# Performance work log

Hardware: AMD Instinct MI355X
Metric: run time of the kernel (lower is better)

The kernel has to match this reference:

```python
import jax, jax.numpy as jnp
import numpy as np

EMB = 1024
HEADS = 16
HEADSIZE = EMB // HEADS
EPS = 1e-5  # torch LayerNorm default


def _layernorm(x, g, b):
    # normalize over last dim (headsize)
    m = jnp.mean(x, axis=-1, keepdims=True)
    v = jnp.mean((x - m) ** 2, axis=-1, keepdims=True)
    return (x - m) * jax.lax.rsqrt(v + EPS) * g + b


def setup_inputs() -> dict:
    key = jax.random.key(0)
    ks = jax.random.split(key, 6)
    B, T = 4, 2048
    s = 1.0 / np.sqrt(EMB)  # ~ torch Linear init scale
    return {
        "x": jax.random.normal(ks[0], (B, T, EMB), dtype=jnp.float32),
        "Wk": jax.random.normal(ks[1], (EMB, EMB), dtype=jnp.float32) * s,
        "Wq": jax.random.normal(ks[2], (EMB, EMB), dtype=jnp.float32) * s,
        "Wv": jax.random.normal(ks[3], (EMB, EMB), dtype=jnp.float32) * s,
        "Wo": jax.random.normal(ks[4], (EMB, EMB), dtype=jnp.float32) * s,
        "bo": jnp.zeros((EMB,), dtype=jnp.float32),
        "kln_g": jnp.ones((HEADSIZE,), dtype=jnp.float32),
        "kln_b": jnp.zeros((HEADSIZE,), dtype=jnp.float32),
        "qln_g": jnp.ones((HEADSIZE,), dtype=jnp.float32),
        "qln_b": jnp.zeros((HEADSIZE,), dtype=jnp.float32),
    }


def reference(x, Wk, Wq, Wv, Wo, bo, kln_g, kln_b, qln_g, qln_b):
    B, T, E = x.shape
    # projections (torch Linear: y = x @ W.T), split into heads
    k = jnp.einsum("bte,fe->btf", x, Wk).reshape(B, T, HEADS, HEADSIZE)
    q = jnp.einsum("bte,fe->btf", x, Wq).reshape(B, T, HEADS, HEADSIZE)
    v = jnp.einsum("bte,fe->btf", x, Wv).reshape(B, T, HEADS, HEADSIZE)
    # optional per-head layernorm on keys/queries (kqnorm=True)
    k = _layernorm(k, kln_g, kln_b)
    q = _layernorm(q, qln_g, qln_b)
    # note: original scales by emb**-1/4 on each of q and k (total 1/sqrt(emb))
    scale = E ** (-0.25)
    q = q * scale
    k = k * scale
    # full [B, H, T, T] score matrix (faithful to bmm implementation)
    dot = jnp.einsum("bihd,bjhd->bhij", q, k)
    # causal mask: j > i set to -inf (mask_diagonal=False -> offset=1)
    causal = jnp.triu(jnp.ones((T, T), dtype=bool), k=1)
    dot = jnp.where(causal, -jnp.inf, dot)
    att = jax.nn.softmax(dot, axis=-1)
    out = jnp.einsum("bhij,bjhd->bihd", att, v).reshape(B, T, E)
    return jnp.einsum("bte,fe->btf", out, Wo) + bo
```

## Files before the change

kernel.cpp:

```cpp
#include <hip/hip_runtime.h>
#include <hip/hip_bf16.h>
#include <cstdint>

#define EMB 1024
#define HEADS 16
#define HD 64
#define BATCH 4
#define SEQ 2048
#define BT (BATCH*SEQ)
#define LNEPS 1e-5f
#define QK_SCALE 0.17677669529663687f
#define LOG2E 1.4426950408889634f

typedef __bf16 bf16;
typedef __bf16 bf16x8 __attribute__((ext_vector_type(8)));
typedef __bf16 bf16x4 __attribute__((ext_vector_type(4)));
typedef float  f32x4  __attribute__((ext_vector_type(4)));
typedef short  s16x4  __attribute__((ext_vector_type(4)));

typedef const __attribute__((address_space(1))) void* gas_ptr;
typedef __attribute__((address_space(3))) void*       las_ptr;

__device__ __forceinline__ void gld_lds16(const void* g, void* l) {
  __builtin_amdgcn_global_load_lds((gas_ptr)g, (las_ptr)l, 16, 0, 0);
}

__device__ __forceinline__ f32x4 mfma_pv(bf16x4 a, bf16x4 b, f32x4 c) {
  return __builtin_amdgcn_mfma_f32_16x16x16bf16_1k(
      __builtin_bit_cast(s16x4, a), __builtin_bit_cast(s16x4, b), c, 0, 0, 0);
}

__global__ void cvt_all(const float* __restrict__ x,
                        const float* __restrict__ w0, const float* __restrict__ w1,
                        const float* __restrict__ w2, const float* __restrict__ w3,
                        bf16* __restrict__ xb, bf16* __restrict__ wb) {
  const int bid = blockIdx.x;
  if (bid < 8192) {
    int i = bid * 256 + threadIdx.x;
    float4 f = reinterpret_cast<const float4*>(x)[i];
    bf16x4 o = { (bf16)f.x, (bf16)f.y, (bf16)f.z, (bf16)f.w };
    reinterpret_cast<bf16x4*>(xb)[i] = o;
  } else {
    int i = (bid - 8192) * 256 + threadIdx.x;
    int sel = i >> 18;
    int j = i & 262143;
    const float* s = (sel == 0) ? w0 : (sel == 1) ? w1 : (sel == 2) ? w2 : w3;
    float4 f = reinterpret_cast<const float4*>(s)[j];
    bf16x4 o = { (bf16)f.x, (bf16)f.y, (bf16)f.z, (bf16)f.w };
    reinterpret_cast<bf16x4*>(wb)[i] = o;
  }
}

__global__ __launch_bounds__(256, 2) void gemm_kqv(
    const bf16* __restrict__ A, const bf16* __restrict__ Bm,
    bf16* __restrict__ kn, bf16* __restrict__ qn, bf16* __restrict__ vt,
    const float* __restrict__ kg, const float* __restrict__ kb,
    const float* __restrict__ qg, const float* __restrict__ qb)
{
  __shared__ __align__(16) bf16 As[128 * 32];
  __shared__ __align__(16) bf16 Bs[128 * 32];

  const int K = EMB;
  const int t    = threadIdx.x;
  const int lane = t & 63;
  const int wave = t >> 6;
  const int q    = lane >> 4;
  const int ln   = lane & 15;

  const int lid = (int)blockIdx.y * (int)gridDim.x + (int)blockIdx.x;
  const int xcd = lid & 7;
  const int nn  = lid >> 3;
  const int bxr = nn >> 3;
  const int byr = (xcd << 3) | (nn & 7);
  const int m0  = byr * 128;
  const int n0  = bxr * 128;

  const int wm = (wave >> 1) * 64;
  const int wn = (wave & 1) * 64;

  const int r0 = t >> 2;
  const int c0 = (t & 3) << 3;

  f32x4 zero4 = {0.f, 0.f, 0.f, 0.f};
  f32x4 acc[4][4];
#pragma unroll
  for (int i = 0; i < 4; i++)
#pragma unroll
    for (int j = 0; j < 4; j++) acc[i][j] = zero4;

  for (int k0 = 0; k0 < K; k0 += 32) {
    __syncthreads();
    const bf16* ga = A  + (size_t)(m0 + r0) * K + k0 + c0;
    const bf16* gb = Bm + (size_t)(n0 + r0) * K + k0 + c0;
    gld_lds16(ga,                  &As[t * 8]);
    gld_lds16(ga + (size_t)64 * K, &As[t * 8 + 2048]);
    gld_lds16(gb,                  &Bs[t * 8]);
    gld_lds16(gb + (size_t)64 * K, &Bs[t * 8 + 2048]);
    __syncthreads();

    bf16x8 af[4], bfr[4];
#pragma unroll
    for (int mi = 0; mi < 4; mi++)
      af[mi] = *reinterpret_cast<const bf16x8*>(&As[(wm + mi * 16 + ln) * 32 + q * 8]);
#pragma unroll
    for (int ni = 0; ni < 4; ni++)
      bfr[ni] = *reinterpret_cast<const bf16x8*>(&Bs[(wn + ni * 16 + ln) * 32 + q * 8]);
#pragma unroll
    for (int mi = 0; mi < 4; mi++)
#pragma unroll
      for (int ni = 0; ni < 4; ni++)
        acc[mi][ni] = __builtin_amdgcn_mfma_f32_16x16x32_bf16(af[mi], bfr[ni], acc[mi][ni], 0, 0, 0);
  }

  const int sec = n0 >> 10;
  const int cb  = (n0 & 1023) + wn;
  const int h   = cb >> 6;
  const int R0  = m0 + wm;

  if (sec == 2) {
#pragma unroll
    for (int mi = 0; mi < 4; mi++) {
      const int R = R0 + mi * 16 + q * 4;
      const int b = R >> 11, tt = R & 2047;
#pragma unroll
      for (int ni = 0; ni < 4; ni++) {
        const int d = ni * 16 + ln;
        bf16x4 o4 = { (bf16)acc[mi][ni][0], (bf16)acc[mi][ni][1],
                      (bf16)acc[mi][ni][2], (bf16)acc[mi][ni][3] };
        *reinterpret_cast<bf16x4*>(
            &vt[((size_t)(b * HEADS + h) * HD + d) * SEQ + tt]) = o4;
      }
    }
  } else {
    const float scale = sec ? QK_SCALE : (QK_SCALE * LOG2E);
    const float* gp = sec ? qg : kg;
    const float* bp = sec ? qb : kb;
    bf16* outp = sec ? qn : kn;
    float gv[4], bv[4];
#pragma unroll
    for (int ni = 0; ni < 4; ni++) {
      gv[ni] = gp[ni * 16 + ln];
      bv[ni] = bp[ni * 16 + ln] * scale;
    }
#pragma unroll
    for (int mi = 0; mi < 4; mi++) {
#pragma unroll
      for (int r = 0; r < 4; r++) {
        const float x0 = acc[mi][0][r], x1 = acc[mi][1][r];
        const float x2 = acc[mi][2][r], x3 = acc[mi][3][r];
        float s  = (x0 + x1) + (x2 + x3);
        float s2 = (x0 * x0 + x1 * x1) + (x2 * x2 + x3 * x3);
#pragma unroll
        for (int mm = 1; mm < 16; mm <<= 1) {
          s  += __shfl_xor(s,  mm, 64);
          s2 += __shfl_xor(s2, mm, 64);
        }
        const float mean = s * (1.f / 64.f);
        const float rs = rsqrtf(s2 * (1.f / 64.f) - mean * mean + LNEPS) * scale;
        const int R = R0 + mi * 16 + q * 4 + r;
        const int b = R >> 11, tt = R & 2047;
        const size_t o = ((size_t)(b * HEADS + h) * SEQ + tt) * HD + ln;
#pragma unroll
        for (int ni = 0; ni < 4; ni++)
          outp[o + ni * 16] = (bf16)((acc[mi][ni][r] - mean) * rs * gv[ni] + bv[ni]);
      }
    }
  }
}

template<int OUTF32>
__global__ __launch_bounds__(256, 2) void gemm_bt(
    const bf16* __restrict__ A, const bf16* __restrict__ Bm,
    bf16* __restrict__ Cb, float* __restrict__ Cf, const float* __restrict__ bias,
    int M, int N, int K)
{
  __shared__ __align__(16) bf16 As[128 * 32];
  __shared__ __align__(16) bf16 Bs[128 * 32];

  const int t    = threadIdx.x;
  const int lane = t & 63;
  const int wave = t >> 6;
  const int q    = lane >> 4;
  const int ln   = lane & 15;

  const int lid = (int)blockIdx.y * (int)gridDim.x + (int)blockIdx.x;
  const int xcd = lid & 7;
  const int nn  = lid >> 3;
  const int bxr = nn >> 3;
  const int byr = (xcd << 3) | (nn & 7);
  const int m0  = byr * 128;
  const int n0  = bxr * 128;

  const int wm   = (wave >> 1) * 64;
  const int wn   = (wave & 1) * 64;

  const int r0 = t >> 2;
  const int c0 = (t & 3) << 3;

  f32x4 zero4 = {0.f, 0.f, 0.f, 0.f};
  f32x4 acc[4][4];
#pragma unroll
  for (int i = 0; i < 4; i++)
#pragma unroll
    for (int j = 0; j < 4; j++) acc[i][j] = zero4;

  for (int k0 = 0; k0 < K; k0 += 32) {
    __syncthreads();
    const bf16* ga = A  + (size_t)(m0 + r0) * K + k0 + c0;
    const bf16* gb = Bm + (size_t)(n0 + r0) * K + k0 + c0;
    gld_lds16(ga,                  &As[t * 8]);
    gld_lds16(ga + (size_t)64 * K, &As[t * 8 + 2048]);
    gld_lds16(gb,                  &Bs[t * 8]);
    gld_lds16(gb + (size_t)64 * K, &Bs[t * 8 + 2048]);
    __syncthreads();

    bf16x8 af[4], bfr[4];
#pragma unroll
    for (int mi = 0; mi < 4; mi++)
      af[mi] = *reinterpret_cast<const bf16x8*>(&As[(wm + mi * 16 + ln) * 32 + q * 8]);
#pragma unroll
    for (int ni = 0; ni < 4; ni++)
      bfr[ni] = *reinterpret_cast<const bf16x8*>(&Bs[(wn + ni * 16 + ln) * 32 + q * 8]);
#pragma unroll
    for (int mi = 0; mi < 4; mi++)
#pragma unroll
      for (int ni = 0; ni < 4; ni++)
        acc[mi][ni] = __builtin_amdgcn_mfma_f32_16x16x32_bf16(af[mi], bfr[ni], acc[mi][ni], 0, 0, 0);
  }

#pragma unroll
  for (int mi = 0; mi < 4; mi++) {
#pragma unroll
    for (int ni = 0; ni < 4; ni++) {
#pragma unroll
      for (int r = 0; r < 4; r++) {
        int row = m0 + wm + mi * 16 + q * 4 + r;
        int col = n0 + wn + ni * 16 + ln;
        float v = acc[mi][ni][r];
        if (OUTF32) Cf[(size_t)row * N + col] = v + bias[col];
        else        Cb[(size_t)row * N + col] = (bf16)v;
      }
    }
  }
}

__global__ __launch_bounds__(256, 4) void attn(
    const bf16* __restrict__ Qn, const bf16* __restrict__ Kn, const bf16* __restrict__ Vt,
    bf16* __restrict__ O)
{
  __shared__ __align__(16) bf16 Ks[2][64 * 64];
  __shared__ __align__(16) bf16 Vs[2][64 * 64];

  const int id = blockIdx.x;
  const int bh = ((id >> 7) << 3) | (id & 7);
  const int bxi = (id >> 3) & 15;
  const int t = threadIdx.x, wave = t >> 6, lane = t & 63;
  const int q = lane >> 4, ln = lane & 15;
  const int b = bh >> 4, h = bh & 15;

  const int u0 = t * 8, u1 = t * 8 + 2048;
  const int kr0 = u0 >> 6, kc0 = ((u0 >> 3) & 7) ^ (kr0 & 7);
  const int kr1 = u1 >> 6, kc1 = ((u1 >> 3) & 7) ^ (kr1 & 7);
  const int vd0 = u0 >> 6, vc0 = ((u0 >> 3) & 7) ^ (vd0 & 7);
  const int vd1 = u1 >> 6, vc1 = ((u1 >> 3) & 7) ^ (vd1 & 7);
  const bf16* Kb = Kn + (size_t)bh * SEQ * HD;
  const bf16* Vb = Vt + (size_t)bh * HD * SEQ;

  f32x4 zero4 = {0.f, 0.f, 0.f, 0.f};

  for (int pass = 0; pass < 2; ++pass) {
    const int itile = pass ? (31 - bxi) : bxi;
    const int qbase = itile * 64 + wave * 16;

    const bf16* qp = Qn + ((size_t)bh * SEQ + qbase + ln) * HD + q * 8;
    bf16x8 qf0 = *reinterpret_cast<const bf16x8*>(qp);
    bf16x8 qf1 = *reinterpret_cast<const bf16x8*>(qp + 32);

    float lrow = 0.f;
    f32x4 oacc[4];
#pragma unroll
    for (int md = 0; md < 4; md++) oacc[md] = zero4;

    const int nj = itile + 1;

    __syncthreads();
    {
      gld_lds16(Kb + (size_t)kr0 * HD + kc0 * 8, &Ks[0][u0]);
      gld_lds16(Kb + (size_t)kr1 * HD + kc1 * 8, &Ks[0][u1]);
      gld_lds16(Vb + (size_t)vd0 * SEQ + vc0 * 8, &Vs[0][u0]);
      gld_lds16(Vb + (size_t)vd1 * SEQ + vc1 * 8, &Vs[0][u1]);
    }

    for (int jt = 0; jt < nj; ++jt) {
      const int buf = jt & 1;
      const int j0 = jt * 64;
      __syncthreads();
      if (jt + 1 < nj) {
        const int jn = j0 + 64;
        gld_lds16(Kb + (size_t)(jn + kr0) * HD + kc0 * 8, &Ks[buf ^ 1][u0]);
        gld_lds16(Kb + (size_t)(jn + kr1) * HD + kc1 * 8, &Ks[buf ^ 1][u1]);
        gld_lds16(Vb + (size_t)vd0 * SEQ + jn + vc0 * 8, &Vs[buf ^ 1][u0]);
        gld_lds16(Vb + (size_t)vd1 * SEQ + jn + vc1 * 8, &Vs[buf ^ 1][u1]);
      }

#pragma unroll
      for (int jb = 0; jb < 4; ++jb) {
        const int jslab = j0 + jb * 16;
        if (jslab <= qbase + 15) {
          const int rowj = jb * 16 + ln;
          bf16x8 kf0 = *reinterpret_cast<const bf16x8*>(
              &Ks[buf][rowj * 64 + ((q)     ^ (rowj & 7)) * 8]);
          bf16x8 kf1 = *reinterpret_cast<const bf16x8*>(
              &Ks[buf][rowj * 64 + ((4 + q) ^ (rowj & 7)) * 8]);
          f32x4 z = zero4;
          z = __builtin_amdgcn_mfma_f32_16x16x32_bf16(kf0, qf0, z, 0, 0, 0);
          z = __builtin_amdgcn_mfma_f32_16x16x32_bf16(kf1, qf1, z, 0, 0, 0);
          if (jslab + 15 > qbase) {
#pragma unroll
            for (int r = 0; r < 4; r++) {
              int jj = jslab + q * 4 + r;
              int ii = qbase + ln;
              if (jj > ii) z[r] = -1.0e30f;
            }
          }
          float p0 = exp2f(z[0]), p1 = exp2f(z[1]), p2 = exp2f(z[2]), p3 = exp2f(z[3]);
          lrow += (p0 + p1) + (p2 + p3);
          bf16x4 pk = { (bf16)p0, (bf16)p1, (bf16)p2, (bf16)p3 };

#pragma unroll
          for (int md = 0; md < 4; md++) {
            const int rowd = md * 16 + ln;
            const bf16* vp = &Vs[buf][rowd * 64 +
                (((jb * 2 + (q >> 1)) ^ (rowd & 7)) * 8) + (q & 1) * 4];
            bf16x4 vf = *reinterpret_cast<const bf16x4*>(vp);
            oacc[md] = mfma_pv(vf, pk, oacc[md]);
          }
        }
      }
    }

    float s = lrow;
    s += __shfl_xor(s, 16, 64);
    s += __shfl_xor(s, 32, 64);
    const float inv = 1.f / s;
    const int row = qbase + ln;
#pragma unroll
    for (int md = 0; md < 4; md++) {
      bf16x4 o4 = { (bf16)(oacc[md][0] * inv), (bf16)(oacc[md][1] * inv),
                    (bf16)(oacc[md][2] * inv), (bf16)(oacc[md][3] * inv) };
      int col = h * HD + md * 16 + q * 4;
      *reinterpret_cast<bf16x4*>(&O[(size_t)(b * SEQ + row) * EMB + col]) = o4;
    }
  }
}

extern "C" void kernel_launch(void* const* d_in, const int* in_sizes, int n_in,
                              void* d_out, int out_size, void* d_ws, size_t ws_size,
                              hipStream_t stream)
{
  const float* x   = (const float*)d_in[0];
  const float* Wk  = (const float*)d_in[1];
  const float* Wq  = (const float*)d_in[2];
  const float* Wv  = (const float*)d_in[3];
  const float* Wo  = (const float*)d_in[4];
  const float* bo  = (const float*)d_in[5];
  const float* klg = (const float*)d_in[6];
  const float* klb = (const float*)d_in[7];
  const float* qlg = (const float*)d_in[8];
  const float* qlb = (const float*)d_in[9];
  float* out = (float*)d_out;

  char* ws = (char*)d_ws;
  const size_t OFF_XB  = 0;
  const size_t OFF_WB  = OFF_XB  + (size_t)BT * EMB * 2;
  const size_t OFF_KQV = OFF_WB  + (size_t)4 * EMB * EMB * 2;
  const size_t OFF_KN  = OFF_KQV + (size_t)BT * 3 * EMB * 2;
  const size_t OFF_QN  = OFF_KN  + (size_t)BT * EMB * 2;
  const size_t OFF_VT  = OFF_QN  + (size_t)BT * EMB * 2;
  const size_t OFF_END = OFF_VT  + (size_t)BT * EMB * 2;
  if (ws_size < OFF_END) return;

  bf16* xb   = (bf16*)(ws + OFF_XB);
  bf16* wb   = (bf16*)(ws + OFF_WB);
  bf16* kn   = (bf16*)(ws + OFF_KN);
  bf16* qn   = (bf16*)(ws + OFF_QN);
  bf16* vt   = (bf16*)(ws + OFF_VT);
  bf16* ob   = (bf16*)(ws + OFF_KQV);

  cvt_all<<<12288, 256, 0, stream>>>(x, Wk, Wq, Wv, Wo, xb, wb);

  gemm_kqv<<<dim3(3 * EMB / 128, BT / 128), 256, 0, stream>>>(
      xb, wb, kn, qn, vt, klg, klb, qlg, qlb);

  attn<<<dim3(16 * BATCH * HEADS), 256, 0, stream>>>(qn, kn, vt, ob);

  gemm_bt<1><<<dim3(EMB / 128, BT / 128), 256, 0, stream>>>(
      ob, wb + (size_t)3 * EMB * EMB, (bf16*)nullptr, out, bo, BT, EMB, EMB);
}
```

Measured before the change: 267.2 us.

## Double-buffer GEMM K-loop with 64-wide swizzled LDS tiles

Both projection GEMMs now share a macro that double-buffers LDS tiles, prefetching the next K tile with global_load_lds while MFMAs run on the current one, and needs only one barrier per iteration. The K tile grows from 32 to 64 and the LDS layout uses an XOR swizzle on 16-byte chunks to avoid bank conflicts on fragment reads. The goal is to hide global load latency and cut barrier and LDS-conflict overhead. LDS use rises to 64KB per block, which may limit occupancy to one block per CU and reduce latency hiding across blocks.

```diff
diff --git a/kernel.cpp b/kernel.cpp
--- a/kernel.cpp
+++ b/kernel.cpp
@@ -51,16 +51,70 @@
   }
 }
 
+#define GEMM_DBUF_LOOP(A_, B_, K_)                                            \
+  f32x4 zero4 = {0.f, 0.f, 0.f, 0.f};                                         \
+  f32x4 acc[4][4];                                                            \
+  _Pragma("unroll")                                                           \
+  for (int i = 0; i < 4; i++)                                                 \
+    _Pragma("unroll")                                                         \
+    for (int j = 0; j < 4; j++) acc[i][j] = zero4;                            \
+  {                                                                           \
+    _Pragma("unroll")                                                         \
+    for (int i = 0; i < 4; i++) {                                             \
+      const int u = t * 8 + i * 2048;                                         \
+      const int row = u >> 6;                                                 \
+      const int c = ((u >> 3) & 7) ^ (row & 7);                               \
+      gld_lds16(A_ + (size_t)(m0 + row) * K_ + c * 8, &As[0][u]);             \
+      gld_lds16(B_ + (size_t)(n0 + row) * K_ + c * 8, &Bs[0][u]);             \
+    }                                                                         \
+  }                                                                           \
+  for (int kt = 0; kt < K_ / 64; ++kt) {                                      \
+    const int buf = kt & 1;                                                   \
+    __syncthreads();                                                          \
+    if (kt + 1 < K_ / 64) {                                                   \
+      const int k0 = (kt + 1) * 64;                                           \
+      _Pragma("unroll")                                                       \
+      for (int i = 0; i < 4; i++) {                                           \
+        const int u = t * 8 + i * 2048;                                       \
+        const int row = u >> 6;                                               \
+        const int c = ((u >> 3) & 7) ^ (row & 7);                             \
+        gld_lds16(A_ + (size_t)(m0 + row) * K_ + k0 + c * 8, &As[buf^1][u]);  \
+        gld_lds16(B_ + (size_t)(n0 + row) * K_ + k0 + c * 8, &Bs[buf^1][u]);  \
+      }                                                                       \
+    }                                                                         \
+    _Pragma("unroll")                                                         \
+    for (int ks = 0; ks < 2; ++ks) {                                          \
+      bf16x8 af[4], bfr[4];                                                   \
+      _Pragma("unroll")                                                       \
+      for (int mi = 0; mi < 4; mi++) {                                        \
+        const int row = wm + mi * 16 + ln;                                    \
+        af[mi] = *reinterpret_cast<const bf16x8*>(                            \
+            &As[buf][row * 64 + ((ks * 4 + q) ^ (row & 7)) * 8]);             \
+      }                                                                       \
+      _Pragma("unroll")                                                       \
+      for (int ni = 0; ni < 4; ni++) {                                        \
+        const int row = wn + ni * 16 + ln;                                    \
+        bfr[ni] = *reinterpret_cast<const bf16x8*>(                           \
+            &Bs[buf][row * 64 + ((ks * 4 + q) ^ (row & 7)) * 8]);             \
+      }                                                                       \
+      _Pragma("unroll")                                                       \
+      for (int mi = 0; mi < 4; mi++)                                          \
+        _Pragma("unroll")                                                     \
+        for (int ni = 0; ni < 4; ni++)                                        \
+          acc[mi][ni] = __builtin_amdgcn_mfma_f32_16x16x32_bf16(              \
+              af[mi], bfr[ni], acc[mi][ni], 0, 0, 0);                         \
+    }                                                                         \
+  }
+
 __global__ __launch_bounds__(256, 2) void gemm_kqv(
     const bf16* __restrict__ A, const bf16* __restrict__ Bm,
     bf16* __restrict__ kn, bf16* __restrict__ qn, bf16* __restrict__ vt,
     const float* __restrict__ kg, const float* __restrict__ kb,
     const float* __restrict__ qg, const float* __restrict__ qb)
 {
-  __shared__ __align__(16) bf16 As[128 * 32];
-  __shared__ __align__(16) bf16 Bs[128 * 32];
-
-  const int K = EMB;
+  __shared__ __align__(16) bf16 As[2][128 * 64];
+  __shared__ __align__(16) bf16 Bs[2][128 * 64];
+
   const int t    = threadIdx.x;
   const int lane = t & 63;
   const int wave = t >> 6;
@@ -78,39 +132,7 @@
   const int wm = (wave >> 1) * 64;
   const int wn = (wave & 1) * 64;
 
-  const int r0 = t >> 2;
-  const int c0 = (t & 3) << 3;
-
-  f32x4 zero4 = {0.f, 0.f, 0.f, 0.f};
-  f32x4 acc[4][4];
-#pragma unroll
-  for (int i = 0; i < 4; i++)
-#pragma unroll
-    for (int j = 0; j < 4; j++) acc[i][j] = zero4;
-
-  for (int k0 = 0; k0 < K; k0 += 32) {
-    __syncthreads();
-    const bf16* ga = A  + (size_t)(m0 + r0) * K + k0 + c0;
-    const bf16* gb = Bm + (size_t)(n0 + r0) * K + k0 + c0;
-    gld_lds16(ga,                  &As[t * 8]);
-    gld_lds16(ga + (size_t)64 * K, &As[t * 8 + 2048]);
-    gld_lds16(gb,                  &Bs[t * 8]);
-    gld_lds16(gb + (size_t)64 * K, &Bs[t * 8 + 2048]);
-    __syncthreads();
-
-    bf16x8 af[4], bfr[4];
-#pragma unroll
-    for (int mi = 0; mi < 4; mi++)
-      af[mi] = *reinterpret_cast<const bf16x8*>(&As[(wm + mi * 16 + ln) * 32 + q * 8]);
-#pragma unroll
-    for (int ni = 0; ni < 4; ni++)
-      bfr[ni] = *reinterpret_cast<const bf16x8*>(&Bs[(wn + ni * 16 + ln) * 32 + q * 8]);
-#pragma unroll
-    for (int mi = 0; mi < 4; mi++)
-#pragma unroll
-      for (int ni = 0; ni < 4; ni++)
-        acc[mi][ni] = __builtin_amdgcn_mfma_f32_16x16x32_bf16(af[mi], bfr[ni], acc[mi][ni], 0, 0, 0);
-  }
+  GEMM_DBUF_LOOP(A, Bm, EMB)
 
   const int sec = n0 >> 10;
   const int cb  = (n0 & 1023) + wn;
@@ -168,14 +190,12 @@
   }
 }
 
-template<int OUTF32>
-__global__ __launch_bounds__(256, 2) void gemm_bt(
+__global__ __launch_bounds__(256, 2) void gemm_out(
     const bf16* __restrict__ A, const bf16* __restrict__ Bm,
-    bf16* __restrict__ Cb, float* __restrict__ Cf, const float* __restrict__ bias,
-    int M, int N, int K)
+    float* __restrict__ Cf, const float* __restrict__ bias, int N)
 {
-  __shared__ __align__(16) bf16 As[128 * 32];
-  __shared__ __align__(16) bf16 Bs[128 * 32];
+  __shared__ __align__(16) bf16 As[2][128 * 64];
+  __shared__ __align__(16) bf16 Bs[2][128 * 64];
 
   const int t    = threadIdx.x;
   const int lane = t & 63;
@@ -191,42 +211,10 @@
   const int m0  = byr * 128;
   const int n0  = bxr * 128;
 
-  const int wm   = (wave >> 1) * 64;
-  const int wn   = (wave & 1) * 64;
-
-  const int r0 = t >> 2;
-  const int c0 = (t & 3) << 3;
-
-  f32x4 zero4 = {0.f, 0.f, 0.f, 0.f};
-  f32x4 acc[4][4];
-#pragma unroll
-  for (int i = 0; i < 4; i++)
-#pragma unroll
-    for (int j = 0; j < 4; j++) acc[i][j] = zero4;
-
-  for (int k0 = 0; k0 < K; k0 += 32) {
-    __syncthreads();
-    const bf16* ga = A  + (size_t)(m0 + r0) * K + k0 + c0;
-    const bf16* gb = Bm + (size_t)(n0 + r0) * K + k0 + c0;
-    gld_lds16(ga,                  &As[t * 8]);
-    gld_lds16(ga + (size_t)64 * K, &As[t * 8 + 2048]);
-    gld_lds16(gb,                  &Bs[t * 8]);
-    gld_lds16(gb + (size_t)64 * K, &Bs[t * 8 + 2048]);
-    __syncthreads();
-
-    bf16x8 af[4], bfr[4];
-#pragma unroll
-    for (int mi = 0; mi < 4; mi++)
-      af[mi] = *reinterpret_cast<const bf16x8*>(&As[(wm + mi * 16 + ln) * 32 + q * 8]);
-#pragma unroll
-    for (int ni = 0; ni < 4; ni++)
-      bfr[ni] = *reinterpret_cast<const bf16x8*>(&Bs[(wn + ni * 16 + ln) * 32 + q * 8]);
-#pragma unroll
-    for (int mi = 0; mi < 4; mi++)
-#pragma unroll
-      for (int ni = 0; ni < 4; ni++)
-        acc[mi][ni] = __builtin_amdgcn_mfma_f32_16x16x32_bf16(af[mi], bfr[ni], acc[mi][ni], 0, 0, 0);
-  }
+  const int wm = (wave >> 1) * 64;
+  const int wn = (wave & 1) * 64;
+
+  GEMM_DBUF_LOOP(A, Bm, EMB)
 
 #pragma unroll
   for (int mi = 0; mi < 4; mi++) {
@@ -236,9 +224,7 @@
       for (int r = 0; r < 4; r++) {
         int row = m0 + wm + mi * 16 + q * 4 + r;
         int col = n0 + wn + ni * 16 + ln;
-        float v = acc[mi][ni][r];
-        if (OUTF32) Cf[(size_t)row * N + col] = v + bias[col];
-        else        Cb[(size_t)row * N + col] = (bf16)v;
+        Cf[(size_t)row * N + col] = acc[mi][ni][r] + bias[col];
       }
     }
   }
@@ -394,6 +380,6 @@
 
   attn<<<dim3(16 * BATCH * HEADS), 256, 0, stream>>>(qn, kn, vt, ob);
 
-  gemm_bt<1><<<dim3(EMB / 128, BT / 128), 256, 0, stream>>>(
-      ob, wb + (size_t)3 * EMB * EMB, (bf16*)nullptr, out, bo, BT, EMB, EMB);
-}
+  gemm_out<<<dim3(EMB / 128, BT / 128), 256, 0, stream>>>(
+      ob, wb + (size_t)3 * EMB * EMB, out, bo, EMB);
+}
```

Result: faster. 259.1 us (-3.0%).
